# Optimization experiments

Measured on AMD Instinct MI355X. Metric: run time of the kernel, lower is better.

The kernel has to match this reference:

```python
import jax, jax.numpy as jnp
import numpy as np
from jax import lax

B, C, H, W = 8, 64, 112, 112
MID = 256
K = 5
DIL = 2
PAD = 4


def setup_inputs() -> dict:
    key = jax.random.key(0)
    k1, k2, k3, k4, k5 = jax.random.split(key, 5)
    x = jax.random.normal(k1, (B, C, H, W), dtype=jnp.float32)
    # conv1: in_channel -> 256, k=5, dilation=2, pad=4
    w1 = jax.random.normal(k2, (MID, C, K, K), dtype=jnp.float32) * (1.0 / np.sqrt(C * K * K))
    b1 = jax.random.normal(k3, (MID,), dtype=jnp.float32) * 0.01
    # conv2: 256 -> 25, 1x1
    w2 = jax.random.normal(k4, (K * K, MID, 1, 1), dtype=jnp.float32) * (1.0 / np.sqrt(MID))
    b2 = jax.random.normal(k5, (K * K,), dtype=jnp.float32) * 0.01
    return {"x": x, "w1": w1, "b1": b1, "w2": w2, "b2": b2}


def reference(x, w1, b1, w2, b2):
    # attention-weight branch
    k = lax.conv_general_dilated(
        x, w1, window_strides=(1, 1), padding=[(PAD, PAD), (PAD, PAD)],
        rhs_dilation=(DIL, DIL), dimension_numbers=("NCHW", "OIHW", "NCHW"))
    k = k + b1[None, :, None, None]                       # [B, 256, H, W]
    k = jnp.einsum("oi,bihw->bohw", w2[:, :, 0, 0], k) + b2[None, :, None, None]
    k = jax.nn.softmax(k, axis=1)                          # [B, 25, H, W]

    # fused local attention: weighted sum over the 5x5 dilated neighborhood.
    # Equivalent to unfold(x, k=5, dilation=2, pad=4) * k summed over the 25 taps,
    # but never materializes the [B, C, 25, H, W] unfolded tensor.
    xp = jnp.pad(x, ((0, 0), (0, 0), (PAD, PAD), (PAD, PAD)))
    out = jnp.zeros_like(x)
    for idx in range(K * K):
        i, j = divmod(idx, K)
        patch = lax.dynamic_slice(xp, (0, 0, DIL * i, DIL * j), (B, C, H, W))
        out = out + patch * k[:, idx:idx + 1]              # broadcast over C
    return out
```

## Files before the change

kernel.cpp:

```cpp
#include <hip/hip_runtime.h>

#define BATCH 8
#define CH    64
#define HH    112
#define WW    112
#define HW    (HH * WW)
#define NP    (BATCH * HW)
#define TAPS  25
#define MIDC  256
#define PIX   64
#define CPW   16
#define NBLK  (NP / PIX)
#define NXCD  8
#define CPX   (NBLK / NXCD)

#define WEFF_N   (CH * TAPS * TAPS)
#define WEFF_TOT (WEFF_N + TAPS)
__global__ __launch_bounds__(256) void weff_kernel(
    const float* __restrict__ w1, const float* __restrict__ b1,
    const float* __restrict__ w2, const float* __restrict__ b2,
    float* __restrict__ weff, float* __restrict__ beff) {
  __shared__ float part[3][64];
  const int lane  = threadIdx.x & 63;
  const int chunk = threadIdx.x >> 6;
  const int id    = blockIdx.x * 64 + lane;

  float acc = 0.f;
  if (id < WEFF_N) {
    const int tap = id % TAPS;
    const int t2  = id / TAPS;
    const int o   = t2 % TAPS;
    const int c   = t2 / TAPS;
    const float* w2o = w2 + o * MIDC + chunk * 64;
    const float* w1p = w1 + ((size_t)(chunk * 64) * CH + c) * TAPS + tap;
    float a0 = 0.f, a1 = 0.f;
    #pragma unroll 8
    for (int m = 0; m < 64; m += 2) {
      a0 = fmaf(w1p[(size_t)m       * CH * TAPS], w2o[m],     a0);
      a1 = fmaf(w1p[(size_t)(m + 1) * CH * TAPS], w2o[m + 1], a1);
    }
    acc = a0 + a1;
  } else if (id < WEFF_TOT) {
    const int o = id - WEFF_N;
    const float* w2o = w2 + o * MIDC + chunk * 64;
    const float* b1p = b1 + chunk * 64;
    #pragma unroll 8
    for (int m = 0; m < 64; ++m) acc = fmaf(w2o[m], b1p[m], acc);
  }

  if (chunk) part[chunk - 1][lane] = acc;
  __syncthreads();
  if (chunk == 0 && id < WEFF_TOT) {
    float r = acc + part[0][lane] + part[1][lane] + part[2][lane];
    if (id < WEFF_N) {
      const int tap = id % TAPS;
      const int t2  = id / TAPS;
      const int o   = t2 % TAPS;
      const int c   = t2 / TAPS;
      weff[(c * TAPS + tap) * TAPS + o] = r;
    } else {
      beff[id - WEFF_N] = r + b2[id - WEFF_N];
    }
  }
}

__global__ __launch_bounds__(256, 6) void picanet_main(
    const float* __restrict__ x, const float* __restrict__ weff,
    const float* __restrict__ beff, float* __restrict__ out) {
  __shared__ float red[2 * PIX * TAPS];

  const int lane = threadIdx.x & 63;
  const int wave = threadIdx.x >> 6;
  const int c0 = __builtin_amdgcn_readfirstlane(wave * CPW);

  const int lb = (blockIdx.x & (NXCD - 1)) * CPX + (blockIdx.x >> 3);
  const int p  = lb * PIX + lane;
  const int b  = p / HW;
  const int hw = p % HW;
  const int h  = hw / WW;
  const int w  = hw % WW;

  const float* xb = x + (size_t)b * CH * HW + (size_t)c0 * HW;
  const float* wc = weff + (size_t)c0 * (TAPS * TAPS);

  float s[TAPS];
  #pragma unroll
  for (int o = 0; o < TAPS; ++o) s[o] = 0.f;

  #pragma unroll 1
  for (int tap = 0; tap < TAPS; ++tap) {
    int i = tap / 5, j = tap % 5;
    int yy = h + 2 * i - 4;
    int xx = w + 2 * j - 4;
    if (yy >= 0 && yy < HH && xx >= 0 && xx < WW) {
      const float* xp = xb + yy * WW + xx;
      float xv[CPW];
      #pragma unroll
      for (int c = 0; c < CPW; ++c) xv[c] = xp[(size_t)c * HW];
      const float* wt = wc + tap * TAPS;
      #pragma unroll
      for (int c = 0; c < CPW; ++c) {
        const float* wp = wt + c * (TAPS * TAPS);
        #pragma unroll
        for (int o = 0; o < TAPS; ++o) s[o] = fmaf(xv[c], wp[o], s[o]);
      }
    }
  }

  if (wave >= 2) {
    float* dst = red + (wave - 2) * (PIX * TAPS);
    #pragma unroll
    for (int o = 0; o < TAPS; ++o) dst[lane * TAPS + o] = s[o];
  }
  __syncthreads();
  if (wave < 2) {
    const float* srcp = red + wave * (PIX * TAPS);
    #pragma unroll
    for (int o = 0; o < TAPS; ++o) s[o] += srcp[lane * TAPS + o];
  }
  if (wave == 1) {
    float* dst = red + (PIX * TAPS);
    #pragma unroll
    for (int o = 0; o < TAPS; ++o) dst[lane * TAPS + o] = s[o];
  }
  __syncthreads();

  if (wave == 0) {
    const float* srcp = red + (PIX * TAPS);
    float t[TAPS];
    #pragma unroll
    for (int o = 0; o < TAPS; ++o)
      t[o] = s[o] + srcp[lane * TAPS + o] + beff[o];
    float m = t[0];
    #pragma unroll
    for (int o = 1; o < TAPS; ++o) m = fmaxf(m, t[o]);
    float sum = 0.f;
    #pragma unroll
    for (int o = 0; o < TAPS; ++o) { t[o] = __expf(t[o] - m); sum += t[o]; }
    float inv = 1.f / sum;
    #pragma unroll
    for (int o = 0; o < TAPS; ++o) red[lane * TAPS + o] = t[o] * inv;
  }
  __syncthreads();

  float acc[CPW];
  #pragma unroll
  for (int c = 0; c < CPW; ++c) acc[c] = 0.f;

  #pragma unroll 1
  for (int tap = 0; tap < TAPS; ++tap) {
    int i = tap / 5, j = tap % 5;
    int yy = h + 2 * i - 4;
    int xx = w + 2 * j - 4;
    float sv = red[lane * TAPS + tap];
    if (yy >= 0 && yy < HH && xx >= 0 && xx < WW) {
      const float* xp = xb + yy * WW + xx;
      #pragma unroll
      for (int c = 0; c < CPW; ++c)
        acc[c] = fmaf(sv, xp[(size_t)c * HW], acc[c]);
    }
  }

  float* ob = out + (size_t)b * CH * HW + (size_t)c0 * HW + hw;
  #pragma unroll
  for (int c = 0; c < CPW; ++c) ob[c * HW] = acc[c];
}

extern "C" void kernel_launch(void* const* d_in, const int* in_sizes, int n_in,
                              void* d_out, int out_size, void* d_ws, size_t ws_size,
                              hipStream_t stream) {
  const float* x  = (const float*)d_in[0];
  const float* w1 = (const float*)d_in[1];
  const float* b1 = (const float*)d_in[2];
  const float* w2 = (const float*)d_in[3];
  const float* b2 = (const float*)d_in[4];
  float* out  = (float*)d_out;
  float* weff = (float*)d_ws;
  float* beff = weff + WEFF_N;

  weff_kernel<<<(WEFF_TOT + 63) / 64, 256, 0, stream>>>(
      w1, b1, w2, b2, weff, beff);
  picanet_main<<<NBLK, 256, 0, stream>>>(x, weff, beff, out);
}
```

Before: 215.8 us.

## Replace serial wave reduction with redundant per-wave softmax and branchless fully-unrolled gather

Measured after the change: 259.5 us. +20.2%, slower.

```diff
diff --git a/kernel.cpp b/kernel.cpp
--- a/kernel.cpp
+++ b/kernel.cpp
@@ -67,7 +67,7 @@
 __global__ __launch_bounds__(256, 6) void picanet_main(
     const float* __restrict__ x, const float* __restrict__ weff,
     const float* __restrict__ beff, float* __restrict__ out) {
-  __shared__ float red[2 * PIX * TAPS];
+  __shared__ float red[4 * PIX * TAPS];
 
   const int lane = threadIdx.x & 63;
   const int wave = threadIdx.x >> 6;
@@ -107,58 +107,47 @@
     }
   }
 
-  if (wave >= 2) {
-    float* dst = red + (wave - 2) * (PIX * TAPS);
-    #pragma unroll
-    for (int o = 0; o < TAPS; ++o) dst[lane * TAPS + o] = s[o];
-  }
-  __syncthreads();
-  if (wave < 2) {
-    const float* srcp = red + wave * (PIX * TAPS);
-    #pragma unroll
-    for (int o = 0; o < TAPS; ++o) s[o] += srcp[lane * TAPS + o];
-  }
-  if (wave == 1) {
-    float* dst = red + (PIX * TAPS);
-    #pragma unroll
-    for (int o = 0; o < TAPS; ++o) dst[lane * TAPS + o] = s[o];
-  }
+  #pragma unroll
+  for (int o = 0; o < TAPS; ++o) red[(wave * PIX + lane) * TAPS + o] = s[o];
   __syncthreads();
 
-  if (wave == 0) {
-    const float* srcp = red + (PIX * TAPS);
-    float t[TAPS];
-    #pragma unroll
-    for (int o = 0; o < TAPS; ++o)
-      t[o] = s[o] + srcp[lane * TAPS + o] + beff[o];
-    float m = t[0];
-    #pragma unroll
-    for (int o = 1; o < TAPS; ++o) m = fmaxf(m, t[o]);
-    float sum = 0.f;
-    #pragma unroll
-    for (int o = 0; o < TAPS; ++o) { t[o] = __expf(t[o] - m); sum += t[o]; }
-    float inv = 1.f / sum;
-    #pragma unroll
-    for (int o = 0; o < TAPS; ++o) red[lane * TAPS + o] = t[o] * inv;
+  float m = -1e30f;
+  #pragma unroll
+  for (int o = 0; o < TAPS; ++o) {
+    float v = red[lane * TAPS + o] + red[(PIX + lane) * TAPS + o] +
+              red[(2 * PIX + lane) * TAPS + o] +
+              red[(3 * PIX + lane) * TAPS + o] + beff[o];
+    s[o] = v;
+    m = fmaxf(m, v);
   }
-  __syncthreads();
+  float sum = 0.f;
+  #pragma unroll
+  for (int o = 0; o < TAPS; ++o) { s[o] = __expf(s[o] - m); sum += s[o]; }
+  float inv = 1.f / sum;
+  #pragma unroll
+  for (int o = 0; o < TAPS; ++o) {
+    int i = o / 5, j = o % 5;
+    int yy = h + 2 * i - 4;
+    int xx = w + 2 * j - 4;
+    bool ok = (yy >= 0) & (yy < HH) & (xx >= 0) & (xx < WW);
+    s[o] = ok ? s[o] * inv : 0.f;
+  }
 
   float acc[CPW];
   #pragma unroll
   for (int c = 0; c < CPW; ++c) acc[c] = 0.f;
 
-  #pragma unroll 1
-  for (int tap = 0; tap < TAPS; ++tap) {
-    int i = tap / 5, j = tap % 5;
+  #pragma unroll
+  for (int t = 0; t < TAPS; ++t) {
+    int i = t / 5, j = t % 5;
     int yy = h + 2 * i - 4;
     int xx = w + 2 * j - 4;
-    float sv = red[lane * TAPS + tap];
-    if (yy >= 0 && yy < HH && xx >= 0 && xx < WW) {
-      const float* xp = xb + yy * WW + xx;
-      #pragma unroll
-      for (int c = 0; c < CPW; ++c)
-        acc[c] = fmaf(sv, xp[(size_t)c * HW], acc[c]);
-    }
+    bool ok = (yy >= 0) & (yy < HH) & (xx >= 0) & (xx < WW);
+    int offt = ok ? yy * WW + xx : hw;
+    float sv = s[t];
+    #pragma unroll
+    for (int c = 0; c < CPW; ++c)
+      acc[c] = fmaf(sv, xb[(size_t)c * HW + offt], acc[c]);
   }
 
   float* ob = out + (size_t)b * CH * HW + (size_t)c0 * HW + hw;
```

## Stage dilated row windows of x in shared memory for both passes

Applied to the files above, without the earlier changes.

Result: slower. 282.1 us (+30.7%).

```diff
diff --git a/kernel.cpp b/kernel.cpp
--- a/kernel.cpp
+++ b/kernel.cpp
@@ -13,6 +13,7 @@
 #define NBLK  (NP / PIX)
 #define NXCD  8
 #define CPX   (NBLK / NXCD)
+#define WIN   72
 
 #define WEFF_N   (CH * TAPS * TAPS)
 #define WEFF_TOT (WEFF_N + TAPS)
@@ -64,13 +65,15 @@
   }
 }
 
-__global__ __launch_bounds__(256, 6) void picanet_main(
+__global__ __launch_bounds__(256, 5) void picanet_main(
     const float* __restrict__ x, const float* __restrict__ weff,
     const float* __restrict__ beff, float* __restrict__ out) {
+  __shared__ float xw[CH * WIN];
   __shared__ float red[2 * PIX * TAPS];
 
-  const int lane = threadIdx.x & 63;
-  const int wave = threadIdx.x >> 6;
+  const int tid  = threadIdx.x;
+  const int lane = tid & 63;
+  const int wave = tid >> 6;
   const int c0 = __builtin_amdgcn_readfirstlane(wave * CPW);
 
   const int lb = (blockIdx.x & (NXCD - 1)) * CPX + (blockIdx.x >> 3);
@@ -79,30 +82,51 @@
   const int hw = p % HW;
   const int h  = hw / WW;
   const int w  = hw % WW;
-
-  const float* xb = x + (size_t)b * CH * HW + (size_t)c0 * HW;
+  const int hw0 = (lb % (HW / PIX)) * PIX;
+
+  const float* xb = x + (size_t)b * CH * HW;
   const float* wc = weff + (size_t)c0 * (TAPS * TAPS);
 
+  bool colok[5];
+  #pragma unroll
+  for (int j = 0; j < 5; ++j) {
+    int xx = w + 2 * j - 4;
+    colok[j] = (xx >= 0) & (xx < WW);
+  }
+
   float s[TAPS];
   #pragma unroll
   for (int o = 0; o < TAPS; ++o) s[o] = 0.f;
 
   #pragma unroll 1
-  for (int tap = 0; tap < TAPS; ++tap) {
-    int i = tap / 5, j = tap % 5;
-    int yy = h + 2 * i - 4;
-    int xx = w + 2 * j - 4;
-    if (yy >= 0 && yy < HH && xx >= 0 && xx < WW) {
-      const float* xp = xb + yy * WW + xx;
-      float xv[CPW];
-      #pragma unroll
-      for (int c = 0; c < CPW; ++c) xv[c] = xp[(size_t)c * HW];
-      const float* wt = wc + tap * TAPS;
-      #pragma unroll
-      for (int c = 0; c < CPW; ++c) {
-        const float* wp = wt + c * (TAPS * TAPS);
+  for (int i = 0; i < 5; ++i) {
+    const int dy    = 2 * i - 4;
+    const int yy    = h + dy;
+    const bool rowok = (yy >= 0) & (yy < HH);
+    const int base  = hw0 + dy * WW - 4;
+
+    __syncthreads();
+    #pragma unroll
+    for (int k = 0; k < 18; ++k) {
+      int e = tid + k * 256;
+      int c = e / WIN, kk = e - c * WIN;
+      int idx = base + kk;
+      idx = min(max(idx, 0), HW - 1);
+      xw[e] = xb[(size_t)c * HW + idx];
+    }
+    __syncthreads();
+
+    #pragma unroll
+    for (int j = 0; j < 5; ++j) {
+      if (rowok & colok[j]) {
+        const float* wt = wc + (i * 5 + j) * TAPS;
         #pragma unroll
-        for (int o = 0; o < TAPS; ++o) s[o] = fmaf(xv[c], wp[o], s[o]);
+        for (int c = 0; c < CPW; ++c) {
+          float xv = xw[(c0 + c) * WIN + lane + 2 * j];
+          const float* wp = wt + c * (TAPS * TAPS);
+          #pragma unroll
+          for (int o = 0; o < TAPS; ++o) s[o] = fmaf(xv, wp[o], s[o]);
+        }
       }
     }
   }
@@ -141,23 +165,37 @@
     #pragma unroll
     for (int o = 0; o < TAPS; ++o) red[lane * TAPS + o] = t[o] * inv;
   }
-  __syncthreads();
 
   float acc[CPW];
   #pragma unroll
   for (int c = 0; c < CPW; ++c) acc[c] = 0.f;
 
   #pragma unroll 1
-  for (int tap = 0; tap < TAPS; ++tap) {
-    int i = tap / 5, j = tap % 5;
-    int yy = h + 2 * i - 4;
-    int xx = w + 2 * j - 4;
-    float sv = red[lane * TAPS + tap];
-    if (yy >= 0 && yy < HH && xx >= 0 && xx < WW) {
-      const float* xp = xb + yy * WW + xx;
-      #pragma unroll
-      for (int c = 0; c < CPW; ++c)
-        acc[c] = fmaf(sv, xp[(size_t)c * HW], acc[c]);
+  for (int i = 0; i < 5; ++i) {
+    const int dy    = 2 * i - 4;
+    const int yy    = h + dy;
+    const bool rowok = (yy >= 0) & (yy < HH);
+    const int base  = hw0 + dy * WW - 4;
+
+    __syncthreads();
+    #pragma unroll
+    for (int k = 0; k < 18; ++k) {
+      int e = tid + k * 256;
+      int c = e / WIN, kk = e - c * WIN;
+      int idx = base + kk;
+      idx = min(max(idx, 0), HW - 1);
+      xw[e] = xb[(size_t)c * HW + idx];
+    }
+    __syncthreads();
+
+    #pragma unroll
+    for (int j = 0; j < 5; ++j) {
+      if (rowok & colok[j]) {
+        float sv = red[lane * TAPS + (i * 5 + j)];
+        #pragma unroll
+        for (int c = 0; c < CPW; ++c)
+          acc[c] = fmaf(sv, xw[(c0 + c) * WIN + lane + 2 * j], acc[c]);
+      }
     }
   }
 
```
